# Kernel tuning notes

Hardware: AMD Instinct MI355X
Metric: run time of the kernel (lower is better)

## Reference

```python
import jax, jax.numpy as jnp
import numpy as np

TOL = 1e-4
EPS = 1e-8


def sinkhorn(cost):
    # cost: (T, L) float32. Matches torch loop: d0 over rows, d1 over cols.
    cost = jnp.exp(cost)
    T, L = cost.shape
    d0 = jnp.ones((T,), jnp.float32)
    d1 = jnp.ones((L,), jnp.float32)

    def cond(state):
        _, _, err = state
        return err > TOL

    def body(state):
        d0, d1, _ = state
        d0n = (1.0 / T) / (cost @ d1 + EPS)          # sum(d1*cost, axis=1)
        d1n = (1.0 / L) / (d0n @ cost + EPS)         # sum(d0[:,None]*cost, axis=0)
        err = jnp.mean(jnp.abs(d1 - d1n))
        return (d0n, d1n, err)

    d0, d1, _ = jax.lax.while_loop(cond, body, (d0, d1, jnp.float32(1e9)))
    return d1[None, :] * cost * d0[:, None]


def setup_inputs() -> dict:
    key = jax.random.key(0)
    k1, k2 = jax.random.split(key)
    T, H, E, L = 8192, 2048, 8, 16
    x = jax.random.normal(k1, (T, H), dtype=jnp.float32)
    w1 = jax.random.normal(k2, (E, H, L), dtype=jnp.float32) * 0.02
    tokens_per_expert = jnp.full((E,), T // E, dtype=jnp.int32)  # sums to T
    return {"x": x, "w1": w1, "tokens_per_expert": tokens_per_expert, "top_k": 2}


def reference(x, w1, tokens_per_expert, top_k):
    T = x.shape[0]
    E = w1.shape[0]
    # grouped GEMM: token t uses weight slab of its expert (tokens are
    # contiguous per expert, counts given by tokens_per_expert)
    eid = jnp.repeat(jnp.arange(E), tokens_per_expert, total_repeat_length=T)  # (T,)
    logits_all = jnp.einsum('th,ehl->tel', x, w1)                 # (T, E, L)
    logits = jnp.take_along_axis(logits_all, eid[:, None, None], axis=1)[:, 0, :]  # (T, L)

    # training path: Sinkhorn (no-grad in torch) selects indices, softmax gives scores
    norm_logits = sinkhorn(logits.astype(jnp.float32))
    _, indices = jax.lax.top_k(norm_logits, top_k)                # (T, k)
    if top_k == 1:
        act = jax.nn.sigmoid(logits)
    else:
        act = jax.nn.softmax(logits.astype(jnp.float32), axis=-1).astype(logits.dtype)
    scores = jnp.take_along_axis(act, indices, axis=1)            # (T, k)
    return scores, indices
```

## Files before the change

kernel.cpp:

```cpp
#include <hip/hip_runtime.h>

constexpr int T_TOK = 8192;
constexpr int H_DIM = 2048;
constexpr int E_NUM = 8;
constexpr int L_DIM = 16;

constexpr int KSB   = 16;
constexpr int NBLK2 = 8;
constexpr int BLK2  = 256;

constexpr size_t WS_SLAB = 0;
constexpr size_t WS_PB   = 512;

__global__ __launch_bounds__(256) void k1a(const float* __restrict__ x,
                                           const float* __restrict__ w1,
                                           const int* __restrict__ tpe,
                                           float* __restrict__ pbT) {
    const int tid  = threadIdx.x;
    const int sb   = blockIdx.x & 15;
    const int tset = blockIdx.x >> 4;
    const int tokg = tid >> 4;
    const int lg   = (tid >> 2) & 3;
    const int ksub = tid & 3;
    const int h0   = sb * 128;

    __shared__ float xbuf[8192];
    __shared__ float wbuf[128 * 20];

    int e = 0;
    {
        const int tok0 = tset * 64;
        int accum = 0;
        #pragma unroll
        for (int i = 0; i < E_NUM - 1; ++i) {
            accum += tpe[i];
            e += (tok0 >= accum) ? 1 : 0;
        }
    }
    const int e0 = __builtin_amdgcn_readfirstlane(e);

    const float4* wsrc =
        reinterpret_cast<const float4*>(w1 + ((size_t)e0 * H_DIM + h0) * L_DIM);
    const float4 wv0 = wsrc[tid];
    const float4 wv1 = wsrc[256 + tid];

    float4 xv[8];
    #pragma unroll
    for (int k = 0; k < 8; ++k) {
        const int slot = tid + 256 * k;
        const int row  = slot >> 5;
        const int pc   = slot & 31;
        const int lc   = pc ^ (((row >> 2) & 3) << 1);
        xv[k] = *reinterpret_cast<const float4*>(
            x + (size_t)(tset * 64 + row) * H_DIM + h0 + 4 * lc);
    }

    {
        const int h  = tid >> 2;
        const int l0 = (tid & 3) * 4;
        *reinterpret_cast<float4*>(&wbuf[h * 20 + l0])        = wv0;
        *reinterpret_cast<float4*>(&wbuf[(64 + h) * 20 + l0]) = wv1;
    }
    #pragma unroll
    for (int k = 0; k < 8; ++k)
        *reinterpret_cast<float4*>(&xbuf[(tid + 256 * k) * 4]) = xv[k];

    __syncthreads();

    float acc[4][4];
    #pragma unroll
    for (int r = 0; r < 4; ++r)
        #pragma unroll
        for (int q = 0; q < 4; ++q) acc[r][q] = 0.f;

    const int tb = (tokg >> 1) & 1;
    const int kk = ksub ^ ((tokg & 1) << 1);
    const float* xrs[4];
    #pragma unroll
    for (int r = 0; r < 4; ++r)
        xrs[r] = &xbuf[(4 * tokg + r) * 128 + 4 * kk];
    const float* wb = &wbuf[(4 * ksub) * 20 + 4 * lg];

    #pragma unroll
    for (int s = 0; s < 8; ++s) {
        const int xo = ((s ^ tb) << 4);
        float4 xr[4], wj[4];
        #pragma unroll
        for (int r = 0; r < 4; ++r)
            xr[r] = *reinterpret_cast<const float4*>(xrs[r] + xo);
        #pragma unroll
        for (int j = 0; j < 4; ++j)
            wj[j] = *reinterpret_cast<const float4*>(wb + 320 * s + 20 * j);
        #pragma unroll
        for (int r = 0; r < 4; ++r) {
            const float xs[4] = {xr[r].x, xr[r].y, xr[r].z, xr[r].w};
            #pragma unroll
            for (int j = 0; j < 4; ++j) {
                acc[r][0] += xs[j] * wj[j].x;
                acc[r][1] += xs[j] * wj[j].y;
                acc[r][2] += xs[j] * wj[j].z;
                acc[r][3] += xs[j] * wj[j].w;
            }
        }
    }

    __syncthreads();
    float* red = xbuf;
    #pragma unroll
    for (int r = 0; r < 4; ++r)
        #pragma unroll
        for (int q = 0; q < 4; ++q)
            red[ksub * 1088 + (4 * tokg + r) * 17 + 4 * lg + q] = acc[r][q];
    __syncthreads();

    {
        const int l  = tid >> 4;
        const int cc = tid & 15;
        float4 o;
        float* op = &o.x;
        #pragma unroll
        for (int j = 0; j < 4; ++j) {
            const int tok = 4 * cc + j;
            op[j] = red[0 * 1088 + tok * 17 + l] + red[1 * 1088 + tok * 17 + l]
                  + red[2 * 1088 + tok * 17 + l] + red[3 * 1088 + tok * 17 + l];
        }
        *reinterpret_cast<float4*>(
            &pbT[((size_t)(sb * 16 + l) << 13) + tset * 64 + 4 * cc]) = o;
    }
}

__global__ __launch_bounds__(256) void k_sinkhorn(float* __restrict__ ws,
                                                  float* __restrict__ out) {
    unsigned long long* slab = reinterpret_cast<unsigned long long*>(ws + WS_SLAB);
    const float* pbT = ws + WS_PB;

    const int tid  = threadIdx.x;
    const int blk  = blockIdx.x;
    const int wv   = tid >> 6;
    const int lane = tid & 63;

    float c[4][16];
    #pragma unroll
    for (int i = 0; i < 4; ++i)
        #pragma unroll
        for (int l = 0; l < 16; ++l) c[i][l] = 0.f;

    #pragma unroll
    for (int sb = 0; sb < KSB; ++sb) {
        #pragma unroll
        for (int l = 0; l < 16; ++l) {
            const float4 v = *reinterpret_cast<const float4*>(
                pbT + ((size_t)(sb * 16 + l) << 13) + blk * 1024 + 4 * tid);
            c[0][l] += v.x; c[1][l] += v.y; c[2][l] += v.z; c[3][l] += v.w;
        }
    }
    #pragma unroll
    for (int i = 0; i < 4; ++i)
        #pragma unroll
        for (int l = 0; l < 16; ++l) c[i][l] = expf(c[i][l]);

    float d1[16];
    #pragma unroll
    for (int l = 0; l < 16; ++l) d1[l] = 1.f;

    __shared__ float s_wpart[4][16];
    __shared__ float s_bpart[NBLK2][16];
    __shared__ float s_d1n[16];

    float d0n[4] = {0.f, 0.f, 0.f, 0.f};
    float err = 1e9f;
    int it = 0;

    do {
        #pragma unroll
        for (int i = 0; i < 4; ++i) {
            float s = 0.f;
            #pragma unroll
            for (int l = 0; l < 16; ++l) s += c[i][l] * d1[l];
            d0n[i] = (1.f / (float)T_TOK) / (s + 1e-8f);
        }

        float con[16];
        #pragma unroll
        for (int l = 0; l < 16; ++l)
            con[l] = d0n[0] * c[0][l] + d0n[1] * c[1][l]
                   + d0n[2] * c[2][l] + d0n[3] * c[3][l];
        #pragma unroll
        for (int m = 1; m < 64; m <<= 1) {
            #pragma unroll
            for (int l = 0; l < 16; ++l) con[l] += __shfl_xor(con[l], m, 64);
        }
        if (lane == 0) {
            #pragma unroll
            for (int l = 0; l < 16; ++l) s_wpart[wv][l] = con[l];
        }
        __syncthreads();

        const int p = it & 1;
        if (tid < 16) {
            const float bs = s_wpart[0][tid] + s_wpart[1][tid]
                           + s_wpart[2][tid] + s_wpart[3][tid];
            const unsigned long long pv =
                ((unsigned long long)(unsigned)it << 32) |
                (unsigned long long)__float_as_uint(bs);
            __hip_atomic_store(&slab[(size_t)p * 128 + blk * 16 + tid],
                               pv, __ATOMIC_RELAXED, __HIP_MEMORY_SCOPE_AGENT);
        }
        if (tid < NBLK2 * 16) {
            unsigned long long v;
            int spins = 0;
            do {
                v = __hip_atomic_load(&slab[(size_t)p * 128 + tid],
                                      __ATOMIC_RELAXED, __HIP_MEMORY_SCOPE_AGENT);
            } while ((unsigned)(v >> 32) != (unsigned)it && ++spins < (1 << 22));
            s_bpart[tid >> 4][tid & 15] = __uint_as_float((unsigned)(v & 0xffffffffull));
        }
        __syncthreads();

        if (tid < 16) {
            float tot = 0.f;
            #pragma unroll
            for (int b = 0; b < NBLK2; ++b) tot += s_bpart[b][tid];
            s_d1n[tid] = (1.f / (float)L_DIM) / (tot + 1e-8f);
        }
        __syncthreads();

        float esum = 0.f;
        #pragma unroll
        for (int l = 0; l < 16; ++l) {
            const float nv = s_d1n[l];
            esum += fabsf(d1[l] - nv);
            d1[l] = nv;
        }
        err = esum * (1.f / 16.f);
        ++it;
    } while (err > 1e-4f && it < 512);

    #pragma unroll
    for (int i = 0; i < 4; ++i) {
        const int t = blk * 1024 + 4 * tid + i;
        float v1 = -__builtin_inff(), v2 = -__builtin_inff();
        float a1 = 0.f, a2 = 0.f;
        int   i1 = 0, i2 = 0;
        float ssum = 0.f;
        #pragma unroll
        for (int l = 0; l < 16; ++l) {
            ssum += c[i][l];
            const float nv = (d1[l] * c[i][l]) * d0n[i];
            if (nv > v1) { v2 = v1; i2 = i1; a2 = a1; v1 = nv; i1 = l; a1 = c[i][l]; }
            else if (nv > v2) { v2 = nv; i2 = l; a2 = c[i][l]; }
        }
        out[(size_t)t * 2 + 0] = a1 / ssum;
        out[(size_t)t * 2 + 1] = a2 / ssum;
        out[(size_t)2 * T_TOK + (size_t)t * 2 + 0] = (float)i1;
        out[(size_t)2 * T_TOK + (size_t)t * 2 + 1] = (float)i2;
    }
}

extern "C" void kernel_launch(void* const* d_in, const int* in_sizes, int n_in,
                              void* d_out, int out_size, void* d_ws, size_t ws_size,
                              hipStream_t stream) {
    const float* x   = (const float*)d_in[0];
    const float* w1  = (const float*)d_in[1];
    const int*   tpe = (const int*)d_in[2];
    float* ws  = (float*)d_ws;
    float* out = (float*)d_out;

    k1a<<<dim3(128 * KSB), dim3(256), 0, stream>>>(x, w1, tpe, ws + WS_PB);

    {
        void* args[] = { (void*)&ws, (void*)&out };
        hipLaunchCooperativeKernel((void*)k_sinkhorn, dim3(NBLK2), dim3(BLK2),
                                   args, 0, stream);
    }
}
```

Measured before the change: 66.36 us.

## Use 1024-thread Sinkhorn blocks with one token per thread

The Sinkhorn kernel now runs 1024 threads per block, each owning one token's 16 cost values, instead of 256 threads each holding four tokens. This shortens the per-thread serial work in every iteration and spreads the 8192 tokens over more waves. In exchange, each block-level reduction has to combine 16 wave partials instead of 4, and the per-iteration __syncthreads barriers cover more waves. The input loads also change from float4 to scalar loads.

```diff
diff --git a/kernel.cpp b/kernel.cpp
--- a/kernel.cpp
+++ b/kernel.cpp
@@ -7,7 +7,7 @@
 
 constexpr int KSB   = 16;
 constexpr int NBLK2 = 8;
-constexpr int BLK2  = 256;
+constexpr int BLK2  = 1024;
 
 constexpr size_t WS_SLAB = 0;
 constexpr size_t WS_PB   = 512;
@@ -129,62 +129,50 @@
     }
 }
 
-__global__ __launch_bounds__(256) void k_sinkhorn(float* __restrict__ ws,
-                                                  float* __restrict__ out) {
+__global__ __launch_bounds__(1024) void k_sinkhorn(float* __restrict__ ws,
+                                                   float* __restrict__ out) {
     unsigned long long* slab = reinterpret_cast<unsigned long long*>(ws + WS_SLAB);
     const float* pbT = ws + WS_PB;
 
     const int tid  = threadIdx.x;
     const int blk  = blockIdx.x;
+    const int t    = blk * BLK2 + tid;
     const int wv   = tid >> 6;
     const int lane = tid & 63;
 
-    float c[4][16];
-    #pragma unroll
-    for (int i = 0; i < 4; ++i)
-        #pragma unroll
-        for (int l = 0; l < 16; ++l) c[i][l] = 0.f;
-
+    float c[16];
+    #pragma unroll
+    for (int l = 0; l < 16; ++l) c[l] = 0.f;
     #pragma unroll
     for (int sb = 0; sb < KSB; ++sb) {
         #pragma unroll
-        for (int l = 0; l < 16; ++l) {
-            const float4 v = *reinterpret_cast<const float4*>(
-                pbT + ((size_t)(sb * 16 + l) << 13) + blk * 1024 + 4 * tid);
-            c[0][l] += v.x; c[1][l] += v.y; c[2][l] += v.z; c[3][l] += v.w;
-        }
-    }
-    #pragma unroll
-    for (int i = 0; i < 4; ++i)
-        #pragma unroll
-        for (int l = 0; l < 16; ++l) c[i][l] = expf(c[i][l]);
+        for (int l = 0; l < 16; ++l)
+            c[l] += pbT[((size_t)(sb * 16 + l) << 13) + t];
+    }
+    #pragma unroll
+    for (int l = 0; l < 16; ++l) c[l] = expf(c[l]);
 
     float d1[16];
     #pragma unroll
     for (int l = 0; l < 16; ++l) d1[l] = 1.f;
 
-    __shared__ float s_wpart[4][16];
+    __shared__ float s_wpart[16][16];
     __shared__ float s_bpart[NBLK2][16];
     __shared__ float s_d1n[16];
 
-    float d0n[4] = {0.f, 0.f, 0.f, 0.f};
+    float d0n = 0.f;
     float err = 1e9f;
     int it = 0;
 
     do {
-        #pragma unroll
-        for (int i = 0; i < 4; ++i) {
-            float s = 0.f;
-            #pragma unroll
-            for (int l = 0; l < 16; ++l) s += c[i][l] * d1[l];
-            d0n[i] = (1.f / (float)T_TOK) / (s + 1e-8f);
-        }
+        float s = 0.f;
+        #pragma unroll
+        for (int l = 0; l < 16; ++l) s += c[l] * d1[l];
+        d0n = (1.f / (float)T_TOK) / (s + 1e-8f);
 
         float con[16];
         #pragma unroll
-        for (int l = 0; l < 16; ++l)
-            con[l] = d0n[0] * c[0][l] + d0n[1] * c[1][l]
-                   + d0n[2] * c[2][l] + d0n[3] * c[3][l];
+        for (int l = 0; l < 16; ++l) con[l] = d0n * c[l];
         #pragma unroll
         for (int m = 1; m < 64; m <<= 1) {
             #pragma unroll
@@ -198,8 +186,9 @@
 
         const int p = it & 1;
         if (tid < 16) {
-            const float bs = s_wpart[0][tid] + s_wpart[1][tid]
-                           + s_wpart[2][tid] + s_wpart[3][tid];
+            float bs = 0.f;
+            #pragma unroll
+            for (int w = 0; w < 16; ++w) bs += s_wpart[w][tid];
             const unsigned long long pv =
                 ((unsigned long long)(unsigned)it << 32) |
                 (unsigned long long)__float_as_uint(bs);
@@ -236,19 +225,17 @@
         ++it;
     } while (err > 1e-4f && it < 512);
 
-    #pragma unroll
-    for (int i = 0; i < 4; ++i) {
-        const int t = blk * 1024 + 4 * tid + i;
+    {
         float v1 = -__builtin_inff(), v2 = -__builtin_inff();
         float a1 = 0.f, a2 = 0.f;
         int   i1 = 0, i2 = 0;
         float ssum = 0.f;
         #pragma unroll
         for (int l = 0; l < 16; ++l) {
-            ssum += c[i][l];
-            const float nv = (d1[l] * c[i][l]) * d0n[i];
-            if (nv > v1) { v2 = v1; i2 = i1; a2 = a1; v1 = nv; i1 = l; a1 = c[i][l]; }
-            else if (nv > v2) { v2 = nv; i2 = l; a2 = c[i][l]; }
+            ssum += c[l];
+            const float nv = (d1[l] * c[l]) * d0n;
+            if (nv > v1) { v2 = v1; i2 = i1; a2 = a1; v1 = nv; i1 = l; a1 = c[l]; }
+            else if (nv > v2) { v2 = nv; i2 = l; a2 = c[l]; }
         }
         out[(size_t)t * 2 + 0] = a1 / ssum;
         out[(size_t)t * 2 + 1] = a2 / ssum;
```

Measured after the change: 128.0 us. +93.0%, slower.
